# Kernel optimization log

Hardware: AMD Instinct MI355X
Metric: run time of the kernel (lower is better)

The kernel has to match this reference:

```python
import jax, jax.numpy as jnp
import numpy as np

N_NODES = 50000


def gcn_conv(x, W, b, src, dst, n_nodes):
    # PyG GCNConv: y = D^-1/2 (A + I) D^-1/2 (x @ W) + b, with D counting self-loops
    h = x @ W                                             # [N, out]
    deg = jnp.ones((n_nodes,), h.dtype).at[dst].add(1.0)  # in-degree + self-loop
    dinv = jax.lax.rsqrt(deg)
    norm = dinv[src] * dinv[dst]                          # [E]
    msg = h[src] * norm[:, None]                          # [E, out]
    out = jnp.zeros_like(h).at[dst].add(msg)              # scatter-add over edges
    out = out + h * (dinv * dinv)[:, None]                # self-loop contribution
    return out + b


def setup_inputs() -> dict:
    key = jax.random.key(0)
    k = jax.random.split(key, 7)
    d_in, d_hid, d_out = 128, 128, 64
    x = jax.random.normal(k[0], (N_NODES, d_in), jnp.float32)
    edge_index = jax.random.randint(k[1], (2, 800000), 0, N_NODES, jnp.int64)
    s1 = 1.0 / np.sqrt(d_in)
    s2 = 1.0 / np.sqrt(d_hid)
    W1 = jax.random.uniform(k[2], (d_in, d_hid), jnp.float32, -s1, s1)
    b1 = jnp.zeros((d_hid,), jnp.float32)
    W2 = jax.random.uniform(k[3], (d_hid, d_out), jnp.float32, -s2, s2)
    b2 = jnp.zeros((d_out,), jnp.float32)
    return {"x": x, "edge_index": edge_index, "W1": W1, "b1": b1, "W2": W2, "b2": b2}


def reference(x, edge_index, W1, b1, W2, b2):
    src, dst = edge_index[0], edge_index[1]
    h = jax.nn.relu(gcn_conv(x, W1, b1, src, dst, N_NODES))
    h = gcn_conv(h, W2, b2, src, dst, N_NODES)
    return jax.nn.log_softmax(h, axis=1)
```

## Files before the change

kernel.cpp:

```cpp
#include <hip/hip_runtime.h>
#include <hip/hip_bf16.h>
#include <math.h>


typedef unsigned int uint32;
typedef unsigned short ushort16;
typedef __attribute__((ext_vector_type(8))) short bf16x8;
typedef __attribute__((ext_vector_type(4))) float f32x4;

__device__ inline unsigned short f2bf_rne(float f) {
    uint32 x = __float_as_uint(f);
    uint32 r = (x + 0x7fffu + ((x >> 16) & 1u)) >> 16;
    return (unsigned short)r;
}
__device__ inline uint32 pack_bf16x2(float a, float b) {
    return (uint32)f2bf_rne(a) | ((uint32)f2bf_rne(b) << 16);
}
__device__ inline float2 unpack_bf16x2(uint32 u) {
    float2 r;
    r.x = __uint_as_float(u << 16);
    r.y = __uint_as_float(u & 0xffff0000u);
    return r;
}

__global__ __launch_bounds__(256) void convw_k(const float* __restrict__ W1,
                                               const float* __restrict__ W2,
                                               unsigned short* __restrict__ W1t,
                                               unsigned short* __restrict__ W2t) {
    int idx = blockIdx.x * 256 + threadIdx.x;
    if (idx < 128 * 128) {
        int ns = idx >> 7, k = idx & 127;
        int t = ns >> 4, m = ns & 15;
        int col = 32 * (t >> 1) + 2 * m + (t & 1);
        W1t[idx] = f2bf_rne(W1[k * 128 + col]);
    } else {
        int i2 = idx - 128 * 128;
        if (i2 < 64 * 128) {
            int ns = i2 >> 7, k = i2 & 127;
            int t = ns >> 4, m = ns & 15;
            int col = 32 * (t >> 1) + 2 * m + (t & 1);
            W2t[i2] = f2bf_rne(W2[k * 64 + col]);
        }
    }
}

__global__ __launch_bounds__(256) void hist_lds_k(const int* __restrict__ dst, int E,
                                                  int NW, int chunk,
                                                  uint32* __restrict__ counts_pb,
                                                  ushort16* __restrict__ rankx) {
    extern __shared__ uint32 sh[];
    const int tid = threadIdx.x;
    const int b   = blockIdx.x;
    for (int i = tid; i < NW; i += 256) sh[i] = 0;
    __syncthreads();
    const int e0 = b * chunk;
    const int e1 = min(E, e0 + chunk);
    int e = e0 + tid;
    for (; e + 768 < e1; e += 1024) {
        int d0 = dst[e];
        int d1 = dst[e + 256];
        int d2 = dst[e + 512];
        int d3 = dst[e + 768];
        uint32 o0 = atomicAdd(&sh[d0 >> 1], (d0 & 1) ? 0x10000u : 1u);
        uint32 o1 = atomicAdd(&sh[d1 >> 1], (d1 & 1) ? 0x10000u : 1u);
        uint32 o2 = atomicAdd(&sh[d2 >> 1], (d2 & 1) ? 0x10000u : 1u);
        uint32 o3 = atomicAdd(&sh[d3 >> 1], (d3 & 1) ? 0x10000u : 1u);
        rankx[e]       = (ushort16)((d0 & 1) ? (o0 >> 16) : (o0 & 0xffffu));
        rankx[e + 256] = (ushort16)((d1 & 1) ? (o1 >> 16) : (o1 & 0xffffu));
        rankx[e + 512] = (ushort16)((d2 & 1) ? (o2 >> 16) : (o2 & 0xffffu));
        rankx[e + 768] = (ushort16)((d3 & 1) ? (o3 >> 16) : (o3 & 0xffffu));
    }
    for (; e < e1; e += 256) {
        int d = dst[e];
        uint32 o = atomicAdd(&sh[d >> 1], (d & 1) ? 0x10000u : 1u);
        rankx[e] = (ushort16)((d & 1) ? (o >> 16) : (o & 0xffffu));
    }
    __syncthreads();
    uint32* dstp = counts_pb + (size_t)b * NW;
    for (int i = tid; i < NW; i += 256) dstp[i] = sh[i];
}

__global__ __launch_bounds__(256) void scan2_k(const uint32* __restrict__ counts_pb,
                                               int N, int NW,
                                               ushort16* __restrict__ basecum,
                                               int* __restrict__ exscan,
                                               int* __restrict__ blocksum,
                                               float* __restrict__ dinv) {
    __shared__ int sd[256];
    const int tid = threadIdx.x;
    const int n   = blockIdx.x * 256 + tid;
    const int nc  = n < N ? n : N - 1;
    const int w   = nc >> 1;
    const bool hi = (nc & 1) != 0;
    int cum = 0;
    for (int bb = 0; bb < 64; bb += 16) {
        uint32 wv[16];
#pragma unroll
        for (int j = 0; j < 16; ++j)
            wv[j] = counts_pb[(size_t)(bb + j) * NW + w];
#pragma unroll
        for (int j = 0; j < 16; ++j) {
            int c = hi ? (int)(wv[j] >> 16) : (int)(wv[j] & 0xffffu);
            if (n < N) basecum[(size_t)(bb + j) * N + n] = (ushort16)cum;
            cum += c;
        }
    }
    int v = (n < N) ? cum : 0;
    if (n < N) dinv[n] = rsqrtf((float)(v + 1));
    sd[tid] = v;
    __syncthreads();
    for (int off = 1; off < 256; off <<= 1) {
        int t = (tid >= off) ? sd[tid - off] : 0;
        __syncthreads();
        sd[tid] += t;
        __syncthreads();
    }
    if (n < N) exscan[n] = sd[tid] - v;
    if (tid == 255) blocksum[blockIdx.x] = sd[255];
}

__global__ __launch_bounds__(256) void scan_blocksums_k(const int* __restrict__ blocksum, int NB,
                                                        int* __restrict__ blockoff,
                                                        int* __restrict__ offsets_last) {
    __shared__ int sd[256];
    const int tid = threadIdx.x;
    int v = (tid < NB) ? blocksum[tid] : 0;
    sd[tid] = v;
    __syncthreads();
    for (int off = 1; off < 256; off <<= 1) {
        int t = (tid >= off) ? sd[tid - off] : 0;
        __syncthreads();
        sd[tid] += t;
        __syncthreads();
    }
    if (tid < NB) blockoff[tid] = sd[tid] - v;
    if (tid == 255) *offsets_last = sd[255];
}

__global__ __launch_bounds__(256) void finalize_k(const int* __restrict__ exscan,
                                                  const int* __restrict__ blockoff, int N,
                                                  int* __restrict__ offsets) {
    const int gid = blockIdx.x * 256 + threadIdx.x;
    if (gid < N) offsets[gid] = blockoff[blockIdx.x] + exscan[gid];
}

__global__ __launch_bounds__(256) void fill_gemm1_k(const int* __restrict__ src,
                                                    const int* __restrict__ dst, int E,
                                                    int chunk, int N,
                                                    const ushort16* __restrict__ rankx,
                                                    const ushort16* __restrict__ basecum,
                                                    const int* __restrict__ offsets,
                                                    int* __restrict__ csr_src,
                                                    const float* __restrict__ X,
                                                    const unsigned short* __restrict__ Wt,
                                                    const float* __restrict__ dinv,
                                                    uint32* __restrict__ Yu, int Nrows) {
    if ((int)blockIdx.x < 256) {
        const int f  = blockIdx.x;
        const int b  = f >> 2;
        const ushort16* bc = basecum + (size_t)b * N;
        const int q4 = chunk >> 2;
        const int e0 = b * chunk + (f & 3) * q4;
        const int e1 = min(E, e0 + q4);
        int e = e0 + threadIdx.x;
        for (; e + 768 < e1; e += 1024) {
#pragma unroll
            for (int j = 0; j < 4; ++j) {
                int ej = e + j * 256;
                int d = dst[ej];
                int pos = offsets[d] + (int)bc[d] + (int)rankx[ej];
                csr_src[pos] = src[ej];
            }
        }
        for (; e < e1; e += 256) {
            int d = dst[e];
            int pos = offsets[d] + (int)bc[d] + (int)rankx[e];
            csr_src[pos] = src[e];
        }
        return;
    }
    constexpr int NCOL = 128;
    constexpr int NT = NCOL / 16;
    const int tid  = threadIdx.x;
    const int wave = tid >> 6;
    const int lane = tid & 63;
    const int m16  = lane & 15;
    const int q    = lane >> 4;
    const int r0   = ((int)blockIdx.x - 256) * 64 + wave * 16;

    int arow = r0 + m16;
    if (arow >= Nrows) arow = Nrows - 1;

    bf16x8 afrag[4];
#pragma unroll
    for (int kb = 0; kb < 4; ++kb) {
        const float* p = &X[(size_t)arow * 128 + kb * 32 + q * 8];
        float4 u0 = *(const float4*)p;
        float4 u1 = *(const float4*)(p + 4);
        bf16x8 a;
        a[0] = (short)f2bf_rne(u0.x); a[1] = (short)f2bf_rne(u0.y);
        a[2] = (short)f2bf_rne(u0.z); a[3] = (short)f2bf_rne(u0.w);
        a[4] = (short)f2bf_rne(u1.x); a[5] = (short)f2bf_rne(u1.y);
        a[6] = (short)f2bf_rne(u1.z); a[7] = (short)f2bf_rne(u1.w);
        afrag[kb] = a;
    }

    f32x4 acc[NT];
#pragma unroll
    for (int t = 0; t < NT; ++t) acc[t] = (f32x4){0.f, 0.f, 0.f, 0.f};
#pragma unroll
    for (int t = 0; t < NT; ++t) {
        const unsigned short* Bp = &Wt[(size_t)(t * 16 + m16) * 128 + q * 8];
#pragma unroll
        for (int kb = 0; kb < 4; ++kb) {
            bf16x8 bfrag = *(const bf16x8*)&Bp[kb * 32];
            acc[t] = __builtin_amdgcn_mfma_f32_16x16x32_bf16(afrag[kb], bfrag, acc[t], 0, 0, 0);
        }
    }
#pragma unroll
    for (int i = 0; i < 4; ++i) {
        int row = r0 + q * 4 + i;
        if (row < Nrows) {
            float dn = dinv[row];
#pragma unroll
            for (int u = 0; u < NT / 2; ++u)
                Yu[(size_t)row * (NCOL / 2) + u * 16 + m16] =
                    pack_bf16x2(acc[2 * u][i] * dn, acc[2 * u + 1][i] * dn);
        }
    }
}

__global__ __launch_bounds__(256) void mfma_gemm2_k(const unsigned short* __restrict__ X,
                                                    const unsigned short* __restrict__ Wt,
                                                    const float* __restrict__ dinv,
                                                    uint32* __restrict__ Yu, int Nrows) {
    constexpr int NCOL = 64;
    constexpr int NT = NCOL / 16;
    const int tid  = threadIdx.x;
    const int wave = tid >> 6;
    const int lane = tid & 63;
    const int m16  = lane & 15;
    const int q    = lane >> 4;
    const int r0   = blockIdx.x * 64 + wave * 16;

    int arow = r0 + m16;
    if (arow >= Nrows) arow = Nrows - 1;

    bf16x8 afrag[4];
#pragma unroll
    for (int kb = 0; kb < 4; ++kb)
        afrag[kb] = *(const bf16x8*)&X[(size_t)arow * 128 + kb * 32 + q * 8];

    f32x4 acc[NT];
#pragma unroll
    for (int t = 0; t < NT; ++t) acc[t] = (f32x4){0.f, 0.f, 0.f, 0.f};
#pragma unroll
    for (int t = 0; t < NT; ++t) {
        const unsigned short* Bp = &Wt[(size_t)(t * 16 + m16) * 128 + q * 8];
#pragma unroll
        for (int kb = 0; kb < 4; ++kb) {
            bf16x8 bfrag = *(const bf16x8*)&Bp[kb * 32];
            acc[t] = __builtin_amdgcn_mfma_f32_16x16x32_bf16(afrag[kb], bfrag, acc[t], 0, 0, 0);
        }
    }
#pragma unroll
    for (int i = 0; i < 4; ++i) {
        int row = r0 + q * 4 + i;
        if (row < Nrows) {
            float dn = dinv[row];
#pragma unroll
            for (int u = 0; u < NT / 2; ++u)
                Yu[(size_t)row * (NCOL / 2) + u * 16 + m16] =
                    pack_bf16x2(acc[2 * u][i] * dn, acc[2 * u + 1][i] * dn);
        }
    }
}

__global__ __launch_bounds__(256) void agg1_k(const unsigned short* __restrict__ hs,
                                              const int* __restrict__ offsets,
                                              const int* __restrict__ csr_src,
                                              const float* __restrict__ dinv,
                                              const float* __restrict__ b1,
                                              unsigned short* __restrict__ out, int N) {
    const int tid  = threadIdx.x;
    const int node = blockIdx.x * 4 + (tid >> 6);
    const int lane = tid & 63;
    if (node >= N) return;
    const uint32* T = (const uint32*)hs;
    const int start = offsets[node];
    const int end   = offsets[node + 1];
    const float dn  = dinv[node];
    float2 self = unpack_bf16x2(T[(size_t)node * 64 + lane]);
    float ax0 = self.x, ay0 = self.y;
    float ax1 = 0.f, ay1 = 0.f, ax2 = 0.f, ay2 = 0.f, ax3 = 0.f, ay3 = 0.f;
    int p = start;
    for (; p + 3 < end; p += 4) {
        int s0 = csr_src[p];
        int s1 = csr_src[p + 1];
        int s2 = csr_src[p + 2];
        int s3 = csr_src[p + 3];
        float2 f0 = unpack_bf16x2(T[(size_t)s0 * 64 + lane]);
        float2 f1 = unpack_bf16x2(T[(size_t)s1 * 64 + lane]);
        float2 f2 = unpack_bf16x2(T[(size_t)s2 * 64 + lane]);
        float2 f3 = unpack_bf16x2(T[(size_t)s3 * 64 + lane]);
        ax0 += f0.x; ay0 += f0.y;
        ax1 += f1.x; ay1 += f1.y;
        ax2 += f2.x; ay2 += f2.y;
        ax3 += f3.x; ay3 += f3.y;
    }
    for (; p < end; ++p) {
        float2 f = unpack_bf16x2(T[(size_t)csr_src[p] * 64 + lane]);
        ax1 += f.x; ay1 += f.y;
    }
    float2 bb = ((const float2*)b1)[lane];
    float vx = ((ax0 + ax1) + (ax2 + ax3)) * dn + bb.x;
    float vy = ((ay0 + ay1) + (ay2 + ay3)) * dn + bb.y;
    vx = vx > 0.f ? vx : 0.f;
    vy = vy > 0.f ? vy : 0.f;
    ((uint32*)out)[(size_t)node * 64 + lane] = pack_bf16x2(vx, vy);
}

__global__ __launch_bounds__(256) void agg2_k(const unsigned short* __restrict__ hs,
                                              const int* __restrict__ offsets,
                                              const int* __restrict__ csr_src,
                                              const float* __restrict__ dinv,
                                              const float* __restrict__ b2,
                                              float* __restrict__ out, int N) {
    const int tid  = threadIdx.x;
    const int node = blockIdx.x * 8 + (tid >> 5);
    const int l    = tid & 31;
    if (node >= N) return;
    const uint32* T = (const uint32*)hs;
    const int start = offsets[node];
    const int end   = offsets[node + 1];
    const float dn  = dinv[node];
    float2 self = unpack_bf16x2(T[(size_t)node * 32 + l]);
    float ax0 = self.x, ay0 = self.y;
    float ax1 = 0.f, ay1 = 0.f, ax2 = 0.f, ay2 = 0.f, ax3 = 0.f, ay3 = 0.f;
    int p = start;
    for (; p + 3 < end; p += 4) {
        int s0 = csr_src[p];
        int s1 = csr_src[p + 1];
        int s2 = csr_src[p + 2];
        int s3 = csr_src[p + 3];
        float2 f0 = unpack_bf16x2(T[(size_t)s0 * 32 + l]);
        float2 f1 = unpack_bf16x2(T[(size_t)s1 * 32 + l]);
        float2 f2 = unpack_bf16x2(T[(size_t)s2 * 32 + l]);
        float2 f3 = unpack_bf16x2(T[(size_t)s3 * 32 + l]);
        ax0 += f0.x; ay0 += f0.y;
        ax1 += f1.x; ay1 += f1.y;
        ax2 += f2.x; ay2 += f2.y;
        ax3 += f3.x; ay3 += f3.y;
    }
    for (; p < end; ++p) {
        float2 f = unpack_bf16x2(T[(size_t)csr_src[p] * 32 + l]);
        ax1 += f.x; ay1 += f.y;
    }
    float2 bb = ((const float2*)b2)[l];
    float vx = ((ax0 + ax1) + (ax2 + ax3)) * dn + bb.x;
    float vy = ((ay0 + ay1) + (ay2 + ay3)) * dn + bb.y;
    float m = fmaxf(vx, vy);
#pragma unroll
    for (int off = 16; off > 0; off >>= 1) m = fmaxf(m, __shfl_xor(m, off, 64));
    float ex = __expf(vx - m) + __expf(vy - m);
    float ssum = ex;
#pragma unroll
    for (int off = 16; off > 0; off >>= 1) ssum += __shfl_xor(ssum, off, 64);
    float lse = m + __logf(ssum);
    float2 o = {vx - lse, vy - lse};
    ((float2*)out)[(size_t)node * 32 + l] = o;
}

extern "C" void kernel_launch(void* const* d_in, const int* in_sizes, int n_in,
                              void* d_out, int out_size, void* d_ws, size_t ws_size,
                              hipStream_t stream) {
    const float* x  = (const float*)d_in[0];
    const int*   ei = (const int*)d_in[1];
    const float* W1 = (const float*)d_in[2];
    const float* b1 = (const float*)d_in[3];
    const float* W2 = (const float*)d_in[4];
    const float* b2 = (const float*)d_in[5];
    float* out = (float*)d_out;

    const int N = in_sizes[0] / 128;
    const int E = in_sizes[1] / 2;
    const int* src = ei;
    const int* dst = ei + E;
    const int NB = (N + 255) / 256;
    const int NW = (N + 1) / 2;
    const int NHB = 64;
    const int chunk = (E + NHB - 1) / NHB;

    char* ws = (char*)d_ws;
    auto alloc = [&](size_t bytes) -> char* {
        char* p = ws;
        ws += (bytes + 255) & ~(size_t)255;
        return p;
    };
    unsigned short* h1  = (unsigned short*)alloc((size_t)N * 128 * 2);
    unsigned short* h1a = (unsigned short*)alloc((size_t)N * 128 * 2);
    unsigned short* h2  = (unsigned short*)alloc((size_t)N * 64 * 2);
    uint32* counts_pb = (uint32*)alloc((size_t)NHB * NW * 4);
    ushort16* basecum = (ushort16*)alloc((size_t)NHB * N * 2);
    ushort16* rankx   = (ushort16*)alloc((size_t)E * 2);
    int*   csr_src  = (int*)alloc((size_t)E * 4);
    float* dinv     = (float*)alloc((size_t)N * 4);
    int*   exscan   = (int*)alloc((size_t)N * 4);
    int*   blocksum = (int*)alloc((size_t)NB * 4);
    int*   blockoff = (int*)alloc((size_t)NB * 4);
    int*   offsets  = (int*)alloc((size_t)(N + 1) * 4);
    unsigned short* W1t = (unsigned short*)alloc(128 * 128 * 2);
    unsigned short* W2t = (unsigned short*)alloc(64 * 128 * 2);

    const int GB = (N + 63) / 64;

    convw_k<<<(128 * 128 + 64 * 128 + 255) / 256, 256, 0, stream>>>(W1, W2, W1t, W2t);
    hist_lds_k<<<NHB, 256, NW * 4, stream>>>(dst, E, NW, chunk, counts_pb, rankx);
    scan2_k<<<NB, 256, 0, stream>>>(counts_pb, N, NW, basecum, exscan, blocksum, dinv);
    scan_blocksums_k<<<1, 256, 0, stream>>>(blocksum, NB, blockoff, offsets + N);
    finalize_k<<<NB, 256, 0, stream>>>(exscan, blockoff, N, offsets);
    fill_gemm1_k<<<256 + GB, 256, 0, stream>>>(src, dst, E, chunk, N, rankx, basecum,
                                               offsets, csr_src, x, W1t, dinv,
                                               (uint32*)h1, N);
    agg1_k<<<(N + 3) / 4, 256, 0, stream>>>(h1, offsets, csr_src, dinv, b1, h1a, N);
    mfma_gemm2_k<<<GB, 256, 0, stream>>>(h1a, W2t, dinv, (uint32*)h2, N);
    agg2_k<<<(N + 7) / 8, 256, 0, stream>>>(h2, offsets, csr_src, dinv, b2, out, N);
}
```

Before: 215.2 us.

## Fuse weight conversion into histogram, merge scan kernels, use 16-bit CSR indices

Folds the weight transpose/bf16 conversion into the histogram kernel as extra blocks, and merges the block-sum scan with offset finalization so each block recomputes the small scan itself. Together these remove launches from the CSR build. It also doubles the number of histogram blocks (NHB 64→128), with the fill phase split accordingly, and stores CSR source indices as 16-bit values to halve index traffic in both aggregation kernels. The 16-bit indices only work while N stays below 65536. The conversion blocks also request the large dynamic LDS allocation, which can limit co-residency.

```diff
diff --git a/kernel.cpp b/kernel.cpp
--- a/kernel.cpp
+++ b/kernel.cpp
@@ -23,34 +23,37 @@
     return r;
 }
 
-__global__ __launch_bounds__(256) void convw_k(const float* __restrict__ W1,
-                                               const float* __restrict__ W2,
-                                               unsigned short* __restrict__ W1t,
-                                               unsigned short* __restrict__ W2t) {
-    int idx = blockIdx.x * 256 + threadIdx.x;
-    if (idx < 128 * 128) {
-        int ns = idx >> 7, k = idx & 127;
-        int t = ns >> 4, m = ns & 15;
-        int col = 32 * (t >> 1) + 2 * m + (t & 1);
-        W1t[idx] = f2bf_rne(W1[k * 128 + col]);
-    } else {
-        int i2 = idx - 128 * 128;
-        if (i2 < 64 * 128) {
-            int ns = i2 >> 7, k = i2 & 127;
+#define NHB 128
+
+__global__ __launch_bounds__(256) void hist_conv_k(const int* __restrict__ dst, int E,
+                                                   int NW, int chunk,
+                                                   uint32* __restrict__ counts_pb,
+                                                   ushort16* __restrict__ rankx,
+                                                   const float* __restrict__ W1,
+                                                   const float* __restrict__ W2,
+                                                   unsigned short* __restrict__ W1t,
+                                                   unsigned short* __restrict__ W2t) {
+    const int tid = threadIdx.x;
+    if ((int)blockIdx.x >= NHB) {
+        int idx = ((int)blockIdx.x - NHB) * 256 + tid;
+        if (idx < 128 * 128) {
+            int ns = idx >> 7, k = idx & 127;
             int t = ns >> 4, m = ns & 15;
             int col = 32 * (t >> 1) + 2 * m + (t & 1);
-            W2t[i2] = f2bf_rne(W2[k * 64 + col]);
-        }
-    }
-}
-
-__global__ __launch_bounds__(256) void hist_lds_k(const int* __restrict__ dst, int E,
-                                                  int NW, int chunk,
-                                                  uint32* __restrict__ counts_pb,
-                                                  ushort16* __restrict__ rankx) {
+            W1t[idx] = f2bf_rne(W1[k * 128 + col]);
+        } else {
+            int i2 = idx - 128 * 128;
+            if (i2 < 64 * 128) {
+                int ns = i2 >> 7, k = i2 & 127;
+                int t = ns >> 4, m = ns & 15;
+                int col = 32 * (t >> 1) + 2 * m + (t & 1);
+                W2t[i2] = f2bf_rne(W2[k * 64 + col]);
+            }
+        }
+        return;
+    }
     extern __shared__ uint32 sh[];
-    const int tid = threadIdx.x;
-    const int b   = blockIdx.x;
+    const int b = blockIdx.x;
     for (int i = tid; i < NW; i += 256) sh[i] = 0;
     __syncthreads();
     const int e0 = b * chunk;
@@ -93,7 +96,7 @@
     const int w   = nc >> 1;
     const bool hi = (nc & 1) != 0;
     int cum = 0;
-    for (int bb = 0; bb < 64; bb += 16) {
+    for (int bb = 0; bb < NHB; bb += 16) {
         uint32 wv[16];
 #pragma unroll
         for (int j = 0; j < 16; ++j)
@@ -119,10 +122,13 @@
     if (tid == 255) blocksum[blockIdx.x] = sd[255];
 }
 
-__global__ __launch_bounds__(256) void scan_blocksums_k(const int* __restrict__ blocksum, int NB,
-                                                        int* __restrict__ blockoff,
-                                                        int* __restrict__ offsets_last) {
+__global__ __launch_bounds__(256) void blocksums_finalize_k(const int* __restrict__ blocksum,
+                                                            int NB,
+                                                            const int* __restrict__ exscan,
+                                                            int N,
+                                                            int* __restrict__ offsets) {
     __shared__ int sd[256];
+    __shared__ int boff;
     const int tid = threadIdx.x;
     int v = (tid < NB) ? blocksum[tid] : 0;
     sd[tid] = v;
@@ -133,15 +139,11 @@
         sd[tid] += t;
         __syncthreads();
     }
-    if (tid < NB) blockoff[tid] = sd[tid] - v;
-    if (tid == 255) *offsets_last = sd[255];
-}
-
-__global__ __launch_bounds__(256) void finalize_k(const int* __restrict__ exscan,
-                                                  const int* __restrict__ blockoff, int N,
-                                                  int* __restrict__ offsets) {
-    const int gid = blockIdx.x * 256 + threadIdx.x;
-    if (gid < N) offsets[gid] = blockoff[blockIdx.x] + exscan[gid];
+    if (tid == 0) boff = sd[blockIdx.x] - blocksum[blockIdx.x];
+    __syncthreads();
+    const int gid = blockIdx.x * 256 + tid;
+    if (gid < N) offsets[gid] = boff + exscan[gid];
+    if (blockIdx.x == 0 && tid == 0) offsets[N] = sd[255];
 }
 
 __global__ __launch_bounds__(256) void fill_gemm1_k(const int* __restrict__ src,
@@ -150,18 +152,18 @@
                                                     const ushort16* __restrict__ rankx,
                                                     const ushort16* __restrict__ basecum,
                                                     const int* __restrict__ offsets,
-                                                    int* __restrict__ csr_src,
+                                                    ushort16* __restrict__ csr_src,
                                                     const float* __restrict__ X,
                                                     const unsigned short* __restrict__ Wt,
                                                     const float* __restrict__ dinv,
                                                     uint32* __restrict__ Yu, int Nrows) {
     if ((int)blockIdx.x < 256) {
         const int f  = blockIdx.x;
-        const int b  = f >> 2;
+        const int b  = f >> 1;
         const ushort16* bc = basecum + (size_t)b * N;
-        const int q4 = chunk >> 2;
-        const int e0 = b * chunk + (f & 3) * q4;
-        const int e1 = min(E, e0 + q4);
+        const int q2 = chunk >> 1;
+        const int e0 = b * chunk + (f & 1) * q2;
+        const int e1 = min(E, e0 + q2);
         int e = e0 + threadIdx.x;
         for (; e + 768 < e1; e += 1024) {
 #pragma unroll
@@ -169,13 +171,13 @@
                 int ej = e + j * 256;
                 int d = dst[ej];
                 int pos = offsets[d] + (int)bc[d] + (int)rankx[ej];
-                csr_src[pos] = src[ej];
+                csr_src[pos] = (ushort16)src[ej];
             }
         }
         for (; e < e1; e += 256) {
             int d = dst[e];
             int pos = offsets[d] + (int)bc[d] + (int)rankx[e];
-            csr_src[pos] = src[e];
+            csr_src[pos] = (ushort16)src[e];
         }
         return;
     }
@@ -278,7 +280,7 @@
 
 __global__ __launch_bounds__(256) void agg1_k(const unsigned short* __restrict__ hs,
                                               const int* __restrict__ offsets,
-                                              const int* __restrict__ csr_src,
+                                              const ushort16* __restrict__ csr_src,
                                               const float* __restrict__ dinv,
                                               const float* __restrict__ b1,
                                               unsigned short* __restrict__ out, int N) {
@@ -322,7 +324,7 @@
 
 __global__ __launch_bounds__(256) void agg2_k(const unsigned short* __restrict__ hs,
                                               const int* __restrict__ offsets,
-                                              const int* __restrict__ csr_src,
+                                              const ushort16* __restrict__ csr_src,
                                               const float* __restrict__ dinv,
                                               const float* __restrict__ b2,
                                               float* __restrict__ out, int N) {
@@ -388,7 +390,6 @@
     const int* dst = ei + E;
     const int NB = (N + 255) / 256;
     const int NW = (N + 1) / 2;
-    const int NHB = 64;
     const int chunk = (E + NHB - 1) / NHB;
 
     char* ws = (char*)d_ws;
@@ -403,22 +404,21 @@
     uint32* counts_pb = (uint32*)alloc((size_t)NHB * NW * 4);
     ushort16* basecum = (ushort16*)alloc((size_t)NHB * N * 2);
     ushort16* rankx   = (ushort16*)alloc((size_t)E * 2);
-    int*   csr_src  = (int*)alloc((size_t)E * 4);
+    ushort16* csr_src = (ushort16*)alloc((size_t)E * 2);
     float* dinv     = (float*)alloc((size_t)N * 4);
     int*   exscan   = (int*)alloc((size_t)N * 4);
     int*   blocksum = (int*)alloc((size_t)NB * 4);
-    int*   blockoff = (int*)alloc((size_t)NB * 4);
     int*   offsets  = (int*)alloc((size_t)(N + 1) * 4);
     unsigned short* W1t = (unsigned short*)alloc(128 * 128 * 2);
     unsigned short* W2t = (unsigned short*)alloc(64 * 128 * 2);
 
     const int GB = (N + 63) / 64;
-
-    convw_k<<<(128 * 128 + 64 * 128 + 255) / 256, 256, 0, stream>>>(W1, W2, W1t, W2t);
-    hist_lds_k<<<NHB, 256, NW * 4, stream>>>(dst, E, NW, chunk, counts_pb, rankx);
+    const int CB = (128 * 128 + 64 * 128 + 255) / 256;
+
+    hist_conv_k<<<NHB + CB, 256, NW * 4, stream>>>(dst, E, NW, chunk, counts_pb, rankx,
+                                                   W1, W2, W1t, W2t);
     scan2_k<<<NB, 256, 0, stream>>>(counts_pb, N, NW, basecum, exscan, blocksum, dinv);
-    scan_blocksums_k<<<1, 256, 0, stream>>>(blocksum, NB, blockoff, offsets + N);
-    finalize_k<<<NB, 256, 0, stream>>>(exscan, blockoff, N, offsets);
+    blocksums_finalize_k<<<NB, 256, 0, stream>>>(blocksum, NB, exscan, N, offsets);
     fill_gemm1_k<<<256 + GB, 256, 0, stream>>>(src, dst, E, chunk, N, rankx, basecum,
                                                offsets, csr_src, x, W1t, dinv,
                                                (uint32*)h1, N);
```

Result: faster. 209.9 us (-2.5%).
